# Performance work log

Hardware: AMD Instinct MI355X
Metric: run time of the kernel (lower is better)

## Reference

```python
import jax, jax.numpy as jnp
import numpy as np

B, D, E, K = 16384, 1024, 8, 2  # tokens, embed_size, experts, top-k
W_IMPORTANCE = 0.01


def setup_inputs() -> dict:
    key = jax.random.key(0)
    ks = jax.random.split(key, 8)
    s = 1.0 / np.sqrt(D)
    return {
        "x": jax.random.normal(ks[0], (B, D), dtype=jnp.float32),   # fused vision features
        "q": jax.random.normal(ks[1], (B, D), dtype=jnp.float32),   # text features
        # cross-attention (seq_len=1) collapses to V then output projection
        "Wv": jax.random.normal(ks[2], (D, D), dtype=jnp.float32) * s,
        "bv": jnp.zeros((D,), dtype=jnp.float32),
        "Wo": jax.random.normal(ks[3], (D, D), dtype=jnp.float32) * s,
        "bo": jnp.zeros((D,), dtype=jnp.float32),
        # gate linear
        "Wg": jax.random.normal(ks[4], (D, E), dtype=jnp.float32) * s,
        "bg": jnp.zeros((E,), dtype=jnp.float32),
        # experts: Linear -> SiLU -> Linear
        "W1": jax.random.normal(ks[5], (E, D, D), dtype=jnp.float32) * s,
        "b1": jnp.zeros((E, D), dtype=jnp.float32),
        "W2": jax.random.normal(ks[6], (E, D, D), dtype=jnp.float32) * s,
        "b2": jnp.zeros((E, D), dtype=jnp.float32),
    }


def reference(x, q, Wv, bv, Wo, bo, Wg, bg, W1, b1, W2, b2):
    # CrossAttention with q_len = kv_len = 1: softmax over a single key is 1,
    # so attention output = out_proj(V(q)).
    att = (q @ Wv + bv) @ Wo + bo                      # (B, D)
    gate_logits = att @ Wg + bg                        # (B, E)
    gate_prob = jax.nn.softmax(gate_logits, axis=-1)   # eval mode: no noise
    top_w, top_i = jax.lax.top_k(gate_prob, K)         # (B, K)
    top_w = jax.nn.softmax(top_w, axis=-1)             # renormalize over top-k

    y = jnp.zeros_like(x)
    for e in range(E):  # small fixed expert count
        w_e = jnp.sum(jnp.where(top_i == e, top_w, 0.0), axis=-1)  # (B,)
        h = jax.nn.silu(x @ W1[e] + b1[e]) @ W2[e] + b2[e]         # (B, D)
        y = y + w_e[:, None] * h

    importance = gate_prob.sum(axis=0)  # (E,)
    importance_loss = W_IMPORTANCE * (jnp.std(importance, ddof=1) / jnp.mean(importance)) ** 2
    return y, gate_prob, importance_loss
```

## Files before the change

### kernel.cpp

```cpp
#include <hip/hip_runtime.h>
#include <hip/hip_bf16.h>

#define Btok 16384
#define Ddim 1024
#define Eexp 8

typedef __attribute__((ext_vector_type(8))) short short8;
typedef __attribute__((ext_vector_type(4))) float f32x4;

__device__ inline unsigned short f2bf(float f) {
    unsigned int u = __float_as_uint(f);
    unsigned int r = (u + 0x7fffu + ((u >> 16) & 1u)) >> 16;
    return (unsigned short)r;
}

__device__ inline void gload16(const void* g, void* l) {
    __builtin_amdgcn_global_load_lds(
        (const __attribute__((address_space(1))) void*)g,
        (__attribute__((address_space(3))) void*)l, 16, 0, 0);
}

__global__ __launch_bounds__(256) void k_tmp(const float* __restrict__ Wo,
                                             const float* __restrict__ Wg,
                                             float* __restrict__ tmp) {
    int id = blockIdx.x * 256 + threadIdx.x;
    int d = id >> 3, e = id & 7;
    double s = 0.0;
    for (int k = 0; k < Ddim; ++k)
        s += (double)Wo[(long)d * Ddim + k] * (double)Wg[k * Eexp + e];
    tmp[id] = (float)s;
}

__global__ __launch_bounds__(256) void k_wc(const float* __restrict__ Wv,
                                            const float* __restrict__ tmp,
                                            float* __restrict__ WcT) {
    int id = blockIdx.x * 256 + threadIdx.x;
    int d = id >> 3, e = id & 7;
    double s = 0.0;
    for (int k = 0; k < Ddim; ++k)
        s += (double)Wv[(long)d * Ddim + k] * (double)tmp[k * Eexp + e];
    WcT[e * Ddim + d] = (float)s;
}

__global__ __launch_bounds__(512) void k_bc(const float* __restrict__ bv,
                                            const float* __restrict__ bo,
                                            const float* __restrict__ bg,
                                            const float* __restrict__ Wg,
                                            const float* __restrict__ tmp,
                                            float* __restrict__ bcomb) {
    int w = threadIdx.x >> 6, l = threadIdx.x & 63;
    double s = 0.0;
    for (int k = l; k < Ddim; k += 64)
        s += (double)bv[k] * (double)tmp[k * Eexp + w] +
             (double)bo[k] * (double)Wg[k * Eexp + w];
    #pragma unroll
    for (int off = 32; off; off >>= 1) s += __shfl_xor(s, off);
    if (l == 0) bcomb[w] = (float)s + bg[w];
}

__global__ __launch_bounds__(256) void k_convx(const float4* __restrict__ x,
                                               ushort4* __restrict__ xb) {
    int i = blockIdx.x * 256 + threadIdx.x;
    float4 v = x[i];
    ushort4 o;
    o.x = f2bf(v.x); o.y = f2bf(v.y); o.z = f2bf(v.z); o.w = f2bf(v.w);
    xb[i] = o;
}

__global__ __launch_bounds__(256) void k_convw(const float* __restrict__ W1,
                                               const float* __restrict__ W2,
                                               unsigned short* __restrict__ w1bT,
                                               unsigned short* __restrict__ w2bT) {
    __shared__ float tile[32][33];
    int bid = blockIdx.x;
    int arr = bid >> 13;
    int e = (bid >> 10) & 7, bi = (bid >> 5) & 31, bj = bid & 31;
    const float* src = (arr ? W2 : W1) + (long)e * Ddim * Ddim;
    unsigned short* dst = (arr ? w2bT : w1bT) + (long)e * Ddim * Ddim;
    int tr = threadIdx.x >> 5, tc = threadIdx.x & 31;
    #pragma unroll
    for (int i = 0; i < 4; ++i) {
        int dl = tr + i * 8;
        tile[dl][tc] = src[(long)(bi * 32 + dl) * Ddim + bj * 32 + tc];
    }
    __syncthreads();
    #pragma unroll
    for (int i = 0; i < 4; ++i) {
        int nl = tr + i * 8;
        dst[(long)(bj * 32 + nl) * Ddim + bi * 32 + tc] = f2bf(tile[tc][nl]);
    }
}

__global__ __launch_bounds__(256) void k_gate(const float* __restrict__ q,
                                              const float* __restrict__ WcT,
                                              const float* __restrict__ bcomb,
                                              float* __restrict__ gate_prob,
                                              int* __restrict__ choice,
                                              float2* __restrict__ w12,
                                              float* __restrict__ impP) {
    __shared__ float impL[4][8];
    int w = threadIdx.x >> 6, l = threadIdx.x & 63;
    int t = blockIdx.x * 4 + w;
    const float* qr = q + (long)t * Ddim;
    float acc[8] = {0, 0, 0, 0, 0, 0, 0, 0};
    #pragma unroll
    for (int i = 0; i < 4; ++i) {
        float4 qv = *(const float4*)(qr + (i * 64 + l) * 4);
        #pragma unroll
        for (int e = 0; e < 8; ++e) {
            float4 wv = *(const float4*)(WcT + e * Ddim + (i * 64 + l) * 4);
            acc[e] += qv.x * wv.x + qv.y * wv.y + qv.z * wv.z + qv.w * wv.w;
        }
    }
    #pragma unroll
    for (int off = 32; off; off >>= 1)
        #pragma unroll
        for (int e = 0; e < 8; ++e) acc[e] += __shfl_xor(acc[e], off);
    float lg[8], p[8];
    float m = -1e30f;
    #pragma unroll
    for (int e = 0; e < 8; ++e) { lg[e] = acc[e] + bcomb[e]; m = fmaxf(m, lg[e]); }
    float s = 0.f;
    #pragma unroll
    for (int e = 0; e < 8; ++e) { p[e] = expf(lg[e] - m); s += p[e]; }
    float inv = 1.f / s;
    #pragma unroll
    for (int e = 0; e < 8; ++e) p[e] *= inv;
    float p1 = -1.f, p2 = -1.f; int i1 = 0, i2 = 0;
    #pragma unroll
    for (int e = 0; e < 8; ++e) {
        float pe = p[e];
        if (pe > p1) { p2 = p1; i2 = i1; p1 = pe; i1 = e; }
        else if (pe > p2) { p2 = pe; i2 = e; }
    }
    float ee = expf(p2 - p1);
    float wa = 1.f / (1.f + ee);
    float wb = ee / (1.f + ee);
    if (l == 0) {
        #pragma unroll
        for (int e = 0; e < 8; ++e) gate_prob[(long)t * 8 + e] = p[e];
        #pragma unroll
        for (int e = 0; e < 8; ++e) impL[w][e] = p[e];
        choice[t] = i1 | (i2 << 8);
        w12[t] = make_float2(wa, wb);
    }
    __syncthreads();
    if (threadIdx.x < 8)
        impP[blockIdx.x * 8 + threadIdx.x] =
            impL[0][threadIdx.x] + impL[1][threadIdx.x] +
            impL[2][threadIdx.x] + impL[3][threadIdx.x];
}

__global__ __launch_bounds__(256) void k_route(const int* __restrict__ choice,
                                               const float2* __restrict__ w12,
                                               int* __restrict__ counts,
                                               int* __restrict__ tok,
                                               float* __restrict__ wgt) {
    __shared__ int cnt[8];
    __shared__ int base[8];
    if (threadIdx.x < 8) cnt[threadIdx.x] = 0;
    __syncthreads();
    int t = blockIdx.x * 256 + threadIdx.x;
    int ch = choice[t];
    int i1 = ch & 255, i2 = ch >> 8;
    float2 ww = w12[t];
    int lp1 = atomicAdd(&cnt[i1], 1);
    int lp2 = atomicAdd(&cnt[i2], 1);
    __syncthreads();
    if (threadIdx.x < 8)
        base[threadIdx.x] = atomicAdd(&counts[threadIdx.x], cnt[threadIdx.x]);
    __syncthreads();
    int p1 = base[i1] + lp1;
    tok[i1 * Btok + p1] = t; wgt[i1 * Btok + p1] = ww.x;
    int p2 = base[i2] + lp2;
    tok[i2 * Btok + p2] = t; wgt[i2 * Btok + p2] = ww.y;
}

template <int MODE>
__global__ __launch_bounds__(256) void k_gemm(const unsigned short* __restrict__ Abase,
                                              const unsigned short* __restrict__ WT,
                                              const float* __restrict__ bias,
                                              const int* __restrict__ counts,
                                              const int* __restrict__ tok,
                                              const float* __restrict__ wgt,
                                              unsigned short* __restrict__ Hout,
                                              float* __restrict__ y) {
    __shared__ unsigned short Ab[128 * 32];
    __shared__ unsigned short Bb[128 * 32];
    int bid = blockIdx.x;
    int ct = bid & 7, rt = (bid >> 3) & 127, e = bid >> 10;
    int n_e = counts[e];
    int r0 = rt * 128;
    if (r0 >= n_e) return;
    int off_e = 0;
    #pragma unroll
    for (int j = 0; j < 8; ++j) off_e += (j < e) ? counts[j] : 0;
    int n0 = ct * 128;
    int t = threadIdx.x;
    int w = t >> 6, l = t & 63;
    int wm = w >> 1, wn = w & 1;

    const char* srcA[2]; const char* srcB[2];
    char* dstA[2]; char* dstB[2];
    #pragma unroll
    for (int i = 0; i < 2; ++i) {
        int row_l = i * 64 + (t >> 2);
        int chunk = t & 3;
        int idx = r0 + row_l; if (idx > n_e - 1) idx = n_e - 1;
        long g = (MODE == 0) ? (long)tok[e * Btok + idx] : (long)(off_e + idx);
        srcA[i] = (const char*)(Abase + g * Ddim + chunk * 8);
        srcB[i] = (const char*)(WT + ((long)e << 20) + (long)(n0 + row_l) * Ddim + chunk * 8);
        dstA[i] = (char*)Ab + i * 4096 + w * 1024;
        dstB[i] = (char*)Bb + i * 4096 + w * 1024;
    }
    f32x4 acc[4][4];
    #pragma unroll
    for (int m = 0; m < 4; ++m)
        #pragma unroll
        for (int n = 0; n < 4; ++n) acc[m][n] = {0.f, 0.f, 0.f, 0.f};

    for (int kk = 0; kk < Ddim; kk += 32) {
        gload16(srcA[0], dstA[0]); gload16(srcA[1], dstA[1]);
        gload16(srcB[0], dstB[0]); gload16(srcB[1], dstB[1]);
        srcA[0] += 64; srcA[1] += 64; srcB[0] += 64; srcB[1] += 64;
        __syncthreads();
        short8 av[4], bv[4];
        #pragma unroll
        for (int m = 0; m < 4; ++m)
            av[m] = *(const short8*)((const char*)Ab +
                     ((wm * 64 + m * 16 + (l & 15)) * 32 + (l >> 4) * 8) * 2);
        #pragma unroll
        for (int n = 0; n < 4; ++n)
            bv[n] = *(const short8*)((const char*)Bb +
                     ((wn * 64 + n * 16 + (l & 15)) * 32 + (l >> 4) * 8) * 2);
        #pragma unroll
        for (int m = 0; m < 4; ++m)
            #pragma unroll
            for (int n = 0; n < 4; ++n)
                acc[m][n] = __builtin_amdgcn_mfma_f32_16x16x32_bf16(av[m], bv[n], acc[m][n], 0, 0, 0);
        __syncthreads();
    }

    #pragma unroll
    for (int m = 0; m < 4; ++m) {
        #pragma unroll
        for (int j = 0; j < 4; ++j) {
            int rl = wm * 64 + m * 16 + (l >> 4) * 4 + j;
            int r = r0 + rl;
            bool ok = r < n_e;
            int trow = 0; float wr = 0.f;
            if (MODE == 1) {
                int ri = ok ? r : 0;
                trow = tok[e * Btok + ri];
                wr = wgt[e * Btok + ri];
            }
            #pragma unroll
            for (int n = 0; n < 4; ++n) {
                int col = n0 + wn * 64 + n * 16 + (l & 15);
                float v = acc[m][n][j] + bias[e * Ddim + col];
                if (MODE == 0) {
                    v = v / (1.f + __expf(-v));
                    if (ok) Hout[(long)(off_e + r) * Ddim + col] = f2bf(v);
                } else {
                    if (ok) atomicAdd(&y[(long)trow * Ddim + col], wr * v);
                }
            }
        }
    }
}

__global__ __launch_bounds__(256) void k_loss(const float* __restrict__ impP,
                                              float* __restrict__ out) {
    __shared__ float red[256];
    __shared__ float impF[8];
    for (int e = 0; e < 8; ++e) {
        float s = 0.f;
        for (int i = threadIdx.x; i < 4096; i += 256) s += impP[i * 8 + e];
        red[threadIdx.x] = s;
        __syncthreads();
        for (int st = 128; st > 0; st >>= 1) {
            if ((int)threadIdx.x < st) red[threadIdx.x] += red[threadIdx.x + st];
            __syncthreads();
        }
        if (threadIdx.x == 0) impF[e] = red[0];
        __syncthreads();
    }
    if (threadIdx.x == 0) {
        double mean = 0.0;
        for (int e = 0; e < 8; ++e) mean += (double)impF[e];
        mean /= 8.0;
        double var = 0.0;
        for (int e = 0; e < 8; ++e) {
            double d = (double)impF[e] - mean;
            var += d * d;
        }
        var /= 7.0;
        out[0] = (float)(0.01 * var / (mean * mean));
    }
}

extern "C" void kernel_launch(void* const* d_in, const int* in_sizes, int n_in,
                              void* d_out, int out_size, void* d_ws, size_t ws_size,
                              hipStream_t stream) {
    const float* x  = (const float*)d_in[0];
    const float* q  = (const float*)d_in[1];
    const float* Wv = (const float*)d_in[2];
    const float* bv = (const float*)d_in[3];
    const float* Wo = (const float*)d_in[4];
    const float* bo = (const float*)d_in[5];
    const float* Wg = (const float*)d_in[6];
    const float* bg = (const float*)d_in[7];
    const float* W1 = (const float*)d_in[8];
    const float* b1 = (const float*)d_in[9];
    const float* W2 = (const float*)d_in[10];
    const float* b2 = (const float*)d_in[11];

    float* y = (float*)d_out;
    float* gate_prob = y + (long)Btok * Ddim;
    float* loss = gate_prob + (long)Btok * Eexp;

    char* ws = (char*)d_ws;
    int*   counts = (int*)(ws + 0);
    float* bcomb  = (float*)(ws + 256);
    float* tmp    = (float*)(ws + 512);
    float* WcT    = (float*)(ws + 33280);
    float* impP   = (float*)(ws + 66048);
    int*   choice = (int*)(ws + 197120);
    float2* w12   = (float2*)(ws + 262656);
    int*   tok    = (int*)(ws + 393728);
    float* wgt    = (float*)(ws + 918016);
    unsigned short* xb   = (unsigned short*)(ws + 1442304);
    unsigned short* w1bT = (unsigned short*)(ws + 34996736);
    unsigned short* w2bT = (unsigned short*)(ws + 51773952);
    unsigned short* H    = (unsigned short*)(ws + 68551168);

    hipMemsetAsync(counts, 0, 32, stream);
    hipMemsetAsync(y, 0, (size_t)Btok * Ddim * sizeof(float), stream);

    k_tmp<<<32, 256, 0, stream>>>(Wo, Wg, tmp);
    k_wc <<<32, 256, 0, stream>>>(Wv, tmp, WcT);
    k_bc <<<1, 512, 0, stream>>>(bv, bo, bg, Wg, tmp, bcomb);
    k_convx<<<16384, 256, 0, stream>>>((const float4*)x, (ushort4*)xb);
    k_convw<<<16384, 256, 0, stream>>>(W1, W2, w1bT, w2bT);
    k_gate<<<4096, 256, 0, stream>>>(q, WcT, bcomb, gate_prob, choice, w12, impP);
    k_route<<<64, 256, 0, stream>>>(choice, w12, counts, tok, wgt);
    k_gemm<0><<<8192, 256, 0, stream>>>(xb, w1bT, b1, counts, tok, wgt, H, nullptr);
    k_gemm<1><<<8192, 256, 0, stream>>>(H, w2bT, b2, counts, tok, wgt, nullptr, y);
    k_loss<<<1, 256, 0, stream>>>(impP, loss);
}
```

Before: 554.7 us.

## Enlarge expert GEMM tiles to 256x256 with double-buffered swizzled LDS

Rewrites the grouped expert GEMM to use 256x256 output tiles per 512-thread block with a K-step of 64, in place of 128x128 tiles with a K-step of 32. LDS staging is double-buffered so the next tile's global-to-LDS loads overlap the current MFMA work, and an XOR swizzle is applied to avoid bank conflicts. Block IDs are remapped so that neighbouring blocks share column tiles, and bias is hoisted into registers. This raises arithmetic intensity and cuts barrier count, at the cost of 128KB LDS per block, more accumulator registers (occupancy drops to one block per CU), and coarser handling of ragged per-expert row counts.

```diff
diff --git a/kernel.cpp b/kernel.cpp
--- a/kernel.cpp
+++ b/kernel.cpp
@@ -177,7 +177,7 @@
 }
 
 template <int MODE>
-__global__ __launch_bounds__(256) void k_gemm(const unsigned short* __restrict__ Abase,
+__global__ __launch_bounds__(512) void k_gemm(const unsigned short* __restrict__ Abase,
                                               const unsigned short* __restrict__ WT,
                                               const float* __restrict__ bias,
                                               const int* __restrict__ counts,
@@ -185,67 +185,95 @@
                                               const float* __restrict__ wgt,
                                               unsigned short* __restrict__ Hout,
                                               float* __restrict__ y) {
-    __shared__ unsigned short Ab[128 * 32];
-    __shared__ unsigned short Bb[128 * 32];
+    __shared__ __align__(16) char lds[131072];
+
     int bid = blockIdx.x;
-    int ct = bid & 7, rt = (bid >> 3) & 127, e = bid >> 10;
+    int wg = (bid & 7) * 256 + (bid >> 3);
+    int ct = wg & 3, rt = (wg >> 2) & 63, e = wg >> 8;
+
     int n_e = counts[e];
-    int r0 = rt * 128;
+    int r0 = rt * 256;
     if (r0 >= n_e) return;
     int off_e = 0;
     #pragma unroll
     for (int j = 0; j < 8; ++j) off_e += (j < e) ? counts[j] : 0;
-    int n0 = ct * 128;
+    int n0 = ct * 256;
+
     int t = threadIdx.x;
     int w = t >> 6, l = t & 63;
-    int wm = w >> 1, wn = w & 1;
-
-    const char* srcA[2]; const char* srcB[2];
-    char* dstA[2]; char* dstB[2];
-    #pragma unroll
-    for (int i = 0; i < 2; ++i) {
-        int row_l = i * 64 + (t >> 2);
-        int chunk = t & 3;
-        int idx = r0 + row_l; if (idx > n_e - 1) idx = n_e - 1;
+    int wm = w >> 2, wn = w & 3;
+
+    int tr = t >> 3;
+    int sc = (t & 7) ^ (tr & 7);
+    const char* srcA[4]; const char* srcB[4];
+    #pragma unroll
+    for (int ri = 0; ri < 4; ++ri) {
+        int idx = r0 + ri * 64 + tr; if (idx > n_e - 1) idx = n_e - 1;
         long g = (MODE == 0) ? (long)tok[e * Btok + idx] : (long)(off_e + idx);
-        srcA[i] = (const char*)(Abase + g * Ddim + chunk * 8);
-        srcB[i] = (const char*)(WT + ((long)e << 20) + (long)(n0 + row_l) * Ddim + chunk * 8);
-        dstA[i] = (char*)Ab + i * 4096 + w * 1024;
-        dstB[i] = (char*)Bb + i * 4096 + w * 1024;
-    }
-    f32x4 acc[4][4];
-    #pragma unroll
-    for (int m = 0; m < 4; ++m)
-        #pragma unroll
-        for (int n = 0; n < 4; ++n) acc[m][n] = {0.f, 0.f, 0.f, 0.f};
-
-    for (int kk = 0; kk < Ddim; kk += 32) {
-        gload16(srcA[0], dstA[0]); gload16(srcA[1], dstA[1]);
-        gload16(srcB[0], dstB[0]); gload16(srcB[1], dstB[1]);
-        srcA[0] += 64; srcA[1] += 64; srcB[0] += 64; srcB[1] += 64;
+        srcA[ri] = (const char*)Abase + g * 2048 + sc * 16;
+        srcB[ri] = (const char*)WT + ((long)e << 21) + (long)(n0 + ri * 64 + tr) * 2048 + sc * 16;
+    }
+
+    int rowAb = (wm * 128 + (l & 15)) * 128;
+    int rowBb = (wn * 64 + (l & 15)) * 128;
+    int x0 = (((l >> 4)) ^ (l & 7)) << 4;
+    int x1 = (((l >> 4) + 4) ^ (l & 7)) << 4;
+
+    f32x4 acc[8][4];
+    #pragma unroll
+    for (int mi = 0; mi < 8; ++mi)
+        #pragma unroll
+        for (int ni = 0; ni < 4; ++ni) acc[mi][ni] = {0.f, 0.f, 0.f, 0.f};
+
+    auto stage = [&](int b) {
+        char* ab = (char*)lds + b * 32768;
+        char* bb = (char*)lds + 65536 + b * 32768;
+        #pragma unroll
+        for (int ri = 0; ri < 4; ++ri) {
+            gload16(srcA[ri], ab + ri * 8192 + w * 1024);
+            gload16(srcB[ri], bb + ri * 8192 + w * 1024);
+            srcA[ri] += 128; srcB[ri] += 128;
+        }
+    };
+
+    const int NT = Ddim / 64;
+    stage(0);
+    __syncthreads();
+    int buf = 0;
+    for (int kk = 0; kk < NT; ++kk) {
+        if (kk + 1 < NT) stage(buf ^ 1);
+        const char* Ap = (const char*)lds + buf * 32768;
+        const char* Bp = (const char*)lds + 65536 + buf * 32768;
+        #pragma unroll
+        for (int ks = 0; ks < 2; ++ks) {
+            int xo = ks ? x1 : x0;
+            short8 av[8], bv[4];
+            #pragma unroll
+            for (int mi = 0; mi < 8; ++mi)
+                av[mi] = *(const short8*)(Ap + rowAb + mi * 2048 + xo);
+            #pragma unroll
+            for (int ni = 0; ni < 4; ++ni)
+                bv[ni] = *(const short8*)(Bp + rowBb + ni * 2048 + xo);
+            #pragma unroll
+            for (int mi = 0; mi < 8; ++mi)
+                #pragma unroll
+                for (int ni = 0; ni < 4; ++ni)
+                    acc[mi][ni] = __builtin_amdgcn_mfma_f32_16x16x32_bf16(av[mi], bv[ni], acc[mi][ni], 0, 0, 0);
+        }
         __syncthreads();
-        short8 av[4], bv[4];
-        #pragma unroll
-        for (int m = 0; m < 4; ++m)
-            av[m] = *(const short8*)((const char*)Ab +
-                     ((wm * 64 + m * 16 + (l & 15)) * 32 + (l >> 4) * 8) * 2);
-        #pragma unroll
-        for (int n = 0; n < 4; ++n)
-            bv[n] = *(const short8*)((const char*)Bb +
-                     ((wn * 64 + n * 16 + (l & 15)) * 32 + (l >> 4) * 8) * 2);
-        #pragma unroll
-        for (int m = 0; m < 4; ++m)
-            #pragma unroll
-            for (int n = 0; n < 4; ++n)
-                acc[m][n] = __builtin_amdgcn_mfma_f32_16x16x32_bf16(av[m], bv[n], acc[m][n], 0, 0, 0);
-        __syncthreads();
-    }
-
-    #pragma unroll
-    for (int m = 0; m < 4; ++m) {
+        buf ^= 1;
+    }
+
+    float bias4[4];
+    #pragma unroll
+    for (int ni = 0; ni < 4; ++ni)
+        bias4[ni] = bias[e * Ddim + n0 + wn * 64 + ni * 16 + (l & 15)];
+
+    #pragma unroll
+    for (int mi = 0; mi < 8; ++mi) {
         #pragma unroll
         for (int j = 0; j < 4; ++j) {
-            int rl = wm * 64 + m * 16 + (l >> 4) * 4 + j;
+            int rl = wm * 128 + mi * 16 + (l >> 4) * 4 + j;
             int r = r0 + rl;
             bool ok = r < n_e;
             int trow = 0; float wr = 0.f;
@@ -255,9 +283,9 @@
                 wr = wgt[e * Btok + ri];
             }
             #pragma unroll
-            for (int n = 0; n < 4; ++n) {
-                int col = n0 + wn * 64 + n * 16 + (l & 15);
-                float v = acc[m][n][j] + bias[e * Ddim + col];
+            for (int ni = 0; ni < 4; ++ni) {
+                int col = n0 + wn * 64 + ni * 16 + (l & 15);
+                float v = acc[mi][ni][j] + bias4[ni];
                 if (MODE == 0) {
                     v = v / (1.f + __expf(-v));
                     if (ok) Hout[(long)(off_e + r) * Ddim + col] = f2bf(v);
@@ -344,7 +372,7 @@
     k_convw<<<16384, 256, 0, stream>>>(W1, W2, w1bT, w2bT);
     k_gate<<<4096, 256, 0, stream>>>(q, WcT, bcomb, gate_prob, choice, w12, impP);
     k_route<<<64, 256, 0, stream>>>(choice, w12, counts, tok, wgt);
-    k_gemm<0><<<8192, 256, 0, stream>>>(xb, w1bT, b1, counts, tok, wgt, H, nullptr);
-    k_gemm<1><<<8192, 256, 0, stream>>>(H, w2bT, b2, counts, tok, wgt, nullptr, y);
+    k_gemm<0><<<2048, 512, 0, stream>>>(xb, w1bT, b1, counts, tok, wgt, H, nullptr);
+    k_gemm<1><<<2048, 512, 0, stream>>>(H, w2bT, b2, counts, tok, wgt, nullptr, y);
     k_loss<<<1, 256, 0, stream>>>(impP, loss);
 }
```

After: 507.4 us. 1.09x faster.
